# Performance work log

Measured on AMD Instinct MI355X. Metric: run time of the kernel, lower is better.

Reference implementation:

```python
import jax, jax.numpy as jnp
import numpy as np

N, M, D = 50000, 4, 512

def setup_inputs() -> dict:
    key = jax.random.key(0)
    k1, k2, k3, k4 = jax.random.split(key, 4)
    scale = 1.0 / np.sqrt(D)
    return {
        "gnn_output": jax.random.normal(k1, (N, D), dtype=jnp.float32),
        "modality_latents": jax.random.normal(k2, (N, M, D), dtype=jnp.float32),
        "Wq": jax.random.normal(k3, (D, D), dtype=jnp.float32) * scale,
        "bq": jnp.zeros((D,), dtype=jnp.float32),
        "Wk": jax.random.normal(k4, (M, D, D), dtype=jnp.float32) * scale,
        "bk": jnp.zeros((M, D), dtype=jnp.float32),
    }

def reference(gnn_output, modality_latents, Wq, bq, Wk, bk):
    d = modality_latents.shape[-1]
    # query = Linear(gnn_output): torch Linear is x @ W.T + b
    query = gnn_output @ Wq.T + bq                                   # [N, D]
    # all M key projections as one batched GEMM (fused version of the loop)
    keys = jnp.einsum('nmd,med->nme', modality_latents, Wk) + bk     # [N, M, D]
    scores = jnp.einsum('nd,nmd->nm', query, keys) / jnp.sqrt(jnp.float32(d))
    weights = jax.nn.softmax(scores, axis=1)                          # [N, M]
    fused = jnp.einsum('nm,nmd->nd', weights, modality_latents)       # [N, D]
    return (fused, weights)
```

## Files before the change

kernel.cpp:

```cpp
#include <hip/hip_runtime.h>
#include <hip/hip_cooperative_groups.h>

namespace cg = cooperative_groups;


typedef __bf16 bf16x8 __attribute__((ext_vector_type(8)));
typedef __bf16 bf16x4 __attribute__((ext_vector_type(4)));
typedef float  f32x4  __attribute__((ext_vector_type(4)));

#define NTOK 50000
#define DDIM 512
#define NMOD 4
#define BN   32
#define NBLK ((NTOK + BN - 1) / BN)
#define WOFF ((size_t)NTOK * DDIM)
#define GFLOATS 524288
#define TAIL_T 1525
#define SCALE 0.044194173824159216f

#define SWZ(r, b) ((((r) * 1024) + (b)) ^ (((r) & 7) << 4))

__global__ __launch_bounds__(512, 2) void mono_kernel(
    const float* __restrict__ gnn, const float* __restrict__ lat,
    const float* __restrict__ Wq, const float* __restrict__ bq,
    const float* __restrict__ Wk, const float* __restrict__ bk,
    float* __restrict__ out, float* __restrict__ sc, int defer)
{
    __shared__ __align__(16) char smem[35328];
    const int tid = threadIdx.x;
    const int bid = blockIdx.x;
    const int ngrid = gridDim.x;
    cg::grid_group gg = cg::this_grid();

    float* uP = sc + GFLOATS;
    float* vP = uP + 2048;
    float* cP = vP + 2048;
    float* fP = cP + 4;

    {
        float* ldsA = (float*)smem;
        float* ldsB = (float*)(smem + 16384);
        for (int gb = bid; gb < 512; gb += ngrid) {
            const int m = gb >> 7, ib = gb & 127, eblk = ib >> 4, dpb = ib & 15;
            const int el = tid >> 3, c8 = tid & 7;
            f32x4 ac = {0.f, 0.f, 0.f, 0.f};
            for (int r0 = 0; r0 < DDIM; r0 += 64) {
                __syncthreads();
                #pragma unroll
                for (int it = 0; it < 2; ++it) {
                    int idx = it * 512 + tid, r = idx >> 4, c4 = idx & 15;
                    *(f32x4*)&ldsA[r * 64 + c4 * 4] =
                        *(const f32x4*)&Wk[((size_t)m * DDIM + r0 + r) * DDIM + eblk * 64 + c4 * 4];
                }
                {
                    int r = tid >> 3, c4 = tid & 7;
                    *(f32x4*)&ldsB[r * 32 + c4 * 4] =
                        *(const f32x4*)&Wq[(size_t)(r0 + r) * DDIM + dpb * 32 + c4 * 4];
                }
                __syncthreads();
                for (int r = 0; r < 64; ++r) {
                    float wk = ldsA[r * 64 + el];
                    ac += wk * *(const f32x4*)&ldsB[r * 32 + c8 * 4];
                }
            }
            __bf16* Gw = (__bf16*)sc;
            const int eta = eblk * 4 + (el >> 4);
            const int lam = (c8 >> 1) * 16 + (el & 15);
            size_t abf = ((((size_t)m * 16 + dpb) * 32 + eta) * 64 + lam) * 8
                         + (c8 & 1) * 4;
            bf16x4 o;
            o[0] = (__bf16)ac[0]; o[1] = (__bf16)ac[1];
            o[2] = (__bf16)ac[2]; o[3] = (__bf16)ac[3];
            *(bf16x4*)(Gw + abf) = o;
        }

        if (bid < 32) {
            __syncthreads();
            float* up = (float*)smem;
            float* vp = (float*)smem + 256;
            const int m2 = bid >> 3, dc = bid & 7;
            if (tid < 256) {
                const int dl2 = tid & 63, eg = tid >> 6;
                const int d = dc * 64 + dl2;
                float us = 0.f, vs = 0.f;
                #pragma unroll 4
                for (int e = eg * 128; e < eg * 128 + 128; ++e) {
                    us += Wk[((size_t)m2 * DDIM + e) * DDIM + d] * bq[e];
                    vs += Wq[(size_t)e * DDIM + d] * bk[m2 * DDIM + e];
                }
                up[eg * 64 + dl2] = us; vp[eg * 64 + dl2] = vs;
            }
            __syncthreads();
            if (tid < 64) {
                const int d = dc * 64 + tid;
                float uu = up[tid] + up[64+tid] + up[128+tid] + up[192+tid];
                float vv = vp[tid] + vp[64+tid] + vp[128+tid] + vp[192+tid];
                uP[m2 * DDIM + d] = uu;
                vP[m2 * DDIM + d] = vv;
                float cp = 0.f;
                if (dc == 0) {
                    #pragma unroll
                    for (int i = 0; i < 8; ++i)
                        cp += bq[tid * 8 + i] * bk[m2 * DDIM + tid * 8 + i];
                    #pragma unroll
                    for (int msk = 1; msk < 64; msk <<= 1)
                        cp += __shfl_xor(cp, msk, 64);
                    if (tid == 0) cP[m2] = cp;
                }
                unsigned long long anyb =
                    __ballot((uu != 0.f) || (vv != 0.f) || (cp != 0.f));
                if (tid == 0) fP[bid] = anyb ? 1.f : 0.f;
            }
        }
    }
    gg.sync();

    {
        __bf16* tile  = (__bf16*)smem;
        float* s_part = (float*)(smem + 32768);
        f32x4* wlds   = (f32x4*)(smem + 34816);
        const __bf16* Gp = (const __bf16*)sc;
        const int lane = tid & 63, w = tid >> 6;
        const int g = (lane >> 4) & 3, c = lane & 15;

        bool bias = false;
        for (int i2 = 0; i2 < 32; ++i2) bias |= (fP[i2] != 0.f);
        float cm[4];
        #pragma unroll
        for (int m = 0; m < 4; ++m) cm[m] = cP[m];

        for (int t = bid; t < NBLK; t += ngrid) {
            const int row0 = t * BN;
            const int vrows = (NTOK - row0 < BN) ? (NTOK - row0) : BN;

            {
                const float* src = gnn + (size_t)row0 * DDIM;
                #pragma unroll
                for (int i = 0; i < 8; ++i) {
                    int f4 = i * 512 + tid, r = f4 >> 7, c4 = f4 & 127;
                    f32x4 v = (r < vrows)
                        ? __builtin_nontemporal_load(
                              (const f32x4*)(src + (size_t)r * DDIM + c4 * 4))
                        : (f32x4){0.f, 0.f, 0.f, 0.f};
                    bf16x4 o;
                    o[0] = (__bf16)v[0]; o[1] = (__bf16)v[1];
                    o[2] = (__bf16)v[2]; o[3] = (__bf16)v[3];
                    *(bf16x4*)((char*)tile + SWZ(r, c4 * 8)) = o;
                }
            }
            __syncthreads();

            float sm[4];
            for (int m = 0; m < NMOD; ++m) {
                float p[2][4];
                if (bias) {
                    float v4[4];
                    #pragma unroll
                    for (int j = 0; j < 4; ++j)
                        v4[j] = vP[m * DDIM + w * 64 + j * 16 + c];
                    #pragma unroll
                    for (int rt = 0; rt < 2; ++rt)
                        #pragma unroll
                        for (int reg = 0; reg < 4; ++reg) {
                            int r = rt * 16 + g * 4 + reg;
                            float tacc = 0.f;
                            #pragma unroll
                            for (int j = 0; j < 4; ++j) {
                                int col = w * 64 + j * 16 + c;
                                float xv = (float)*(const __bf16*)((const char*)tile +
                                                                   SWZ(r, col * 2));
                                tacc += xv * v4[j];
                            }
                            p[rt][reg] = tacc;
                        }
                } else {
                    #pragma unroll
                    for (int rt = 0; rt < 2; ++rt)
                        #pragma unroll
                        for (int reg = 0; reg < 4; ++reg)
                            p[rt][reg] = 0.f;
                }

                const __bf16* gm = Gp + (size_t)m * 262144;
                #pragma unroll
                for (int jh = 0; jh < 2; ++jh) {
                    float lv[2][2][4];
                    #pragma unroll
                    for (int jj = 0; jj < 2; ++jj) {
                        const int e = w * 64 + (jh * 2 + jj) * 16 + c;
                        #pragma unroll
                        for (int rt = 0; rt < 2; ++rt)
                            #pragma unroll
                            for (int reg = 0; reg < 4; ++reg) {
                                int row = row0 + rt * 16 + g * 4 + reg;
                                lv[jj][rt][reg] = (row < NTOK)
                                    ? lat[((size_t)row * NMOD + m) * DDIM + e]
                                    : 0.f;
                            }
                    }

                    f32x4 kacc[2][2];
                    #pragma unroll
                    for (int rt = 0; rt < 2; ++rt) {
                        kacc[rt][0] = (f32x4){0.f, 0.f, 0.f, 0.f};
                        kacc[rt][1] = (f32x4){0.f, 0.f, 0.f, 0.f};
                    }
                    const __bf16* gpk = gm + (w * 4 + jh * 2) * 512 + lane * 8;
                    #pragma unroll 4
                    for (int kk = 0; kk < 16; ++kk) {
                        bf16x8 b0 = *(const bf16x8*)(gpk + kk * 16384);
                        bf16x8 b1 = *(const bf16x8*)(gpk + kk * 16384 + 512);
                        bf16x8 a[2];
                        const int kb = kk * 64 + g * 16;
                        a[0] = *(const bf16x8*)((const char*)tile + SWZ(c, kb));
                        a[1] = *(const bf16x8*)((const char*)tile + SWZ(16 + c, kb));
                        kacc[0][0] = __builtin_amdgcn_mfma_f32_16x16x32_bf16(
                            a[0], b0, kacc[0][0], 0, 0, 0);
                        kacc[1][0] = __builtin_amdgcn_mfma_f32_16x16x32_bf16(
                            a[1], b0, kacc[1][0], 0, 0, 0);
                        kacc[0][1] = __builtin_amdgcn_mfma_f32_16x16x32_bf16(
                            a[0], b1, kacc[0][1], 0, 0, 0);
                        kacc[1][1] = __builtin_amdgcn_mfma_f32_16x16x32_bf16(
                            a[1], b1, kacc[1][1], 0, 0, 0);
                    }

                    #pragma unroll
                    for (int jj = 0; jj < 2; ++jj) {
                        const int e = w * 64 + (jh * 2 + jj) * 16 + c;
                        float uj = bias ? uP[m * DDIM + e] : 0.f;
                        #pragma unroll
                        for (int rt = 0; rt < 2; ++rt)
                            #pragma unroll
                            for (int reg = 0; reg < 4; ++reg)
                                p[rt][reg] += lv[jj][rt][reg] * (kacc[rt][jj][reg] + uj);
                    }
                    __builtin_amdgcn_sched_barrier(0);
                }

                #pragma unroll
                for (int msk = 1; msk < 16; msk <<= 1)
                    #pragma unroll
                    for (int rt = 0; rt < 2; ++rt)
                        #pragma unroll
                        for (int reg = 0; reg < 4; ++reg)
                            p[rt][reg] += __shfl_xor(p[rt][reg], msk, 64);
                float* sp = s_part + (m & 1) * 256;
                if (c == 0) {
                    #pragma unroll
                    for (int rt = 0; rt < 2; ++rt)
                        #pragma unroll
                        for (int reg = 0; reg < 4; ++reg)
                            sp[w * 32 + rt * 16 + g * 4 + reg] = p[rt][reg];
                }
                __syncthreads();
                if (tid < BN) {
                    float s = 0.f;
                    #pragma unroll
                    for (int ww = 0; ww < 8; ++ww) s += sp[ww * 32 + tid];
                    sm[m] = s + cm[m];
                }
            }

            if (tid < BN) {
                float e0 = __expf(sm[0] * SCALE), e1 = __expf(sm[1] * SCALE),
                      e2 = __expf(sm[2] * SCALE), e3 = __expf(sm[3] * SCALE);
                float iz = 1.f / (e0 + e1 + e2 + e3);
                f32x4 wv = {e0 * iz, e1 * iz, e2 * iz, e3 * iz};
                wlds[tid] = wv;
                if (row0 + tid < NTOK)
                    *(f32x4*)(out + WOFF + (size_t)(row0 + tid) * 4) = wv;
            }
            __syncthreads();

            if (!defer || t < TAIL_T) {
                #pragma unroll 2
                for (int i = 0; i < 8; ++i) {
                    int f4 = i * 512 + tid, r = f4 >> 7, c4 = f4 & 127;
                    if (row0 + r < NTOK) {
                        f32x4 w4 = wlds[r];
                        const float* lp = lat + (size_t)(row0 + r) * NMOD * DDIM + c4 * 4;
                        f32x4 acc = {0.f, 0.f, 0.f, 0.f};
                        #pragma unroll
                        for (int m = 0; m < NMOD; ++m)
                            acc += w4[m] * *(const f32x4*)(lp + m * DDIM);
                        __builtin_nontemporal_store(acc,
                            (f32x4*)(out + (size_t)(row0 + r) * DDIM + c4 * 4));
                    }
                }
            }
        }
    }

    if (defer) {
        gg.sync();
        const long t4 = (long)(NTOK - TAIL_T * BN) * 128;
        for (long idx = (long)bid * 512 + tid; idx < t4;
             idx += (long)ngrid * 512) {
            const int row = TAIL_T * BN + (int)(idx >> 7), c4 = (int)(idx & 127);
            f32x4 w4 = *(const f32x4*)(out + WOFF + (size_t)row * 4);
            f32x4 acc = {0.f, 0.f, 0.f, 0.f};
            #pragma unroll
            for (int m = 0; m < NMOD; ++m) {
                f32x4 v = __builtin_nontemporal_load(
                    (const f32x4*)(lat + ((size_t)row * NMOD + m) * DDIM + c4 * 4));
                acc += w4[m] * v;
            }
            __builtin_nontemporal_store(acc,
                (f32x4*)(out + (size_t)row * DDIM + c4 * 4));
        }
    }
}

extern "C" void kernel_launch(void* const* d_in, const int* in_sizes, int n_in,
                              void* d_out, int out_size, void* d_ws, size_t ws_size,
                              hipStream_t stream)
{
    const float* gnn = (const float*)d_in[0];
    const float* lat = (const float*)d_in[1];
    const float* Wq  = (const float*)d_in[2];
    const float* bq  = (const float*)d_in[3];
    const float* Wk  = (const float*)d_in[4];
    const float* bk  = (const float*)d_in[5];
    float* out = (float*)d_out;

    const size_t need = (size_t)(GFLOATS + 2048 + 2048 + 4 + 32 + 16) * 4;
    float* sc;
    int defer;
    if (ws_size >= need) { sc = (float*)d_ws;      defer = 0; }
    else                 { sc = out + 25000000;    defer = 1; }

    int maxb = 0;
    hipError_t oe = hipOccupancyMaxActiveBlocksPerMultiprocessor(
        &maxb, mono_kernel, 512, 0);
    if (oe != hipSuccess || maxb < 1) maxb = 1;
    if (maxb > 4) maxb = 4;
    const int ngrid = 256 * maxb;

    void* args[] = { (void*)&gnn, (void*)&lat, (void*)&Wq, (void*)&bq,
                     (void*)&Wk, (void*)&bk, (void*)&out, (void*)&sc,
                     (void*)&defer };
    hipLaunchCooperativeKernel((const void*)mono_kernel, dim3(ngrid), dim3(512),
                               args, 0, stream);
}
```

Baseline: 517.2 us.

## Double token tile to 64 rows and use atomic work queue for tiles

Raises the per-block token tile from 32 to 64 rows, so each streamed bf16 weight fragment feeds four MFMA row tiles instead of two, halving global/L2 traffic for the precomputed Wk·Wq matrix per token. Replaces the static strided tile loop with a dynamic atomic counter queue, which balances the load across persistent blocks. In exchange, LDS per block roughly doubles and register pressure grows, which may reduce occupancy under launch_bounds(512,2). The tail-tile count used in defer mode is adjusted to match.

```diff
diff --git a/kernel.cpp b/kernel.cpp
--- a/kernel.cpp
+++ b/kernel.cpp
@@ -11,11 +11,11 @@
 #define NTOK 50000
 #define DDIM 512
 #define NMOD 4
-#define BN   32
+#define BN   64
 #define NBLK ((NTOK + BN - 1) / BN)
 #define WOFF ((size_t)NTOK * DDIM)
 #define GFLOATS 524288
-#define TAIL_T 1525
+#define TAIL_T 762
 #define SCALE 0.044194173824159216f
 
 #define SWZ(r, b) ((((r) * 1024) + (b)) ^ (((r) & 7) << 4))
@@ -26,7 +26,7 @@
     const float* __restrict__ Wk, const float* __restrict__ bk,
     float* __restrict__ out, float* __restrict__ sc, int defer)
 {
-    __shared__ __align__(16) char smem[35328];
+    __shared__ __align__(16) char smem[70720];
     const int tid = threadIdx.x;
     const int bid = blockIdx.x;
     const int ngrid = gridDim.x;
@@ -36,8 +36,10 @@
     float* vP = uP + 2048;
     float* cP = vP + 2048;
     float* fP = cP + 4;
+    int*   qP = (int*)(fP + 32);
 
     {
+        if (bid == 0 && tid == 0) *qP = 0;
         float* ldsA = (float*)smem;
         float* ldsB = (float*)(smem + 16384);
         for (int gb = bid; gb < 512; gb += ngrid) {
@@ -117,8 +119,9 @@
 
     {
         __bf16* tile  = (__bf16*)smem;
-        float* s_part = (float*)(smem + 32768);
-        f32x4* wlds   = (f32x4*)(smem + 34816);
+        float* s_part = (float*)(smem + 65536);
+        f32x4* wlds   = (f32x4*)(smem + 69632);
+        int*   tlds   = (int*)(smem + 70656);
         const __bf16* Gp = (const __bf16*)sc;
         const int lane = tid & 63, w = tid >> 6;
         const int g = (lane >> 4) & 3, c = lane & 15;
@@ -129,14 +132,18 @@
         #pragma unroll
         for (int m = 0; m < 4; ++m) cm[m] = cP[m];
 
-        for (int t = bid; t < NBLK; t += ngrid) {
+        for (;;) {
+            if (tid == 0) *tlds = atomicAdd(qP, 1);
+            __syncthreads();
+            const int t = *tlds;
+            if (t >= NBLK) break;
             const int row0 = t * BN;
             const int vrows = (NTOK - row0 < BN) ? (NTOK - row0) : BN;
 
             {
                 const float* src = gnn + (size_t)row0 * DDIM;
                 #pragma unroll
-                for (int i = 0; i < 8; ++i) {
+                for (int i = 0; i < 16; ++i) {
                     int f4 = i * 512 + tid, r = f4 >> 7, c4 = f4 & 127;
                     f32x4 v = (r < vrows)
                         ? __builtin_nontemporal_load(
@@ -152,14 +159,14 @@
 
             float sm[4];
             for (int m = 0; m < NMOD; ++m) {
-                float p[2][4];
+                float p[4][4];
                 if (bias) {
                     float v4[4];
                     #pragma unroll
                     for (int j = 0; j < 4; ++j)
                         v4[j] = vP[m * DDIM + w * 64 + j * 16 + c];
                     #pragma unroll
-                    for (int rt = 0; rt < 2; ++rt)
+                    for (int rt = 0; rt < 4; ++rt)
                         #pragma unroll
                         for (int reg = 0; reg < 4; ++reg) {
                             int r = rt * 16 + g * 4 + reg;
@@ -175,7 +182,7 @@
                         }
                 } else {
                     #pragma unroll
-                    for (int rt = 0; rt < 2; ++rt)
+                    for (int rt = 0; rt < 4; ++rt)
                         #pragma unroll
                         for (int reg = 0; reg < 4; ++reg)
                             p[rt][reg] = 0.f;
@@ -183,80 +190,68 @@
 
                 const __bf16* gm = Gp + (size_t)m * 262144;
                 #pragma unroll
-                for (int jh = 0; jh < 2; ++jh) {
-                    float lv[2][2][4];
-                    #pragma unroll
-                    for (int jj = 0; jj < 2; ++jj) {
-                        const int e = w * 64 + (jh * 2 + jj) * 16 + c;
-                        #pragma unroll
-                        for (int rt = 0; rt < 2; ++rt)
-                            #pragma unroll
-                            for (int reg = 0; reg < 4; ++reg) {
-                                int row = row0 + rt * 16 + g * 4 + reg;
-                                lv[jj][rt][reg] = (row < NTOK)
-                                    ? lat[((size_t)row * NMOD + m) * DDIM + e]
-                                    : 0.f;
-                            }
+                for (int jp = 0; jp < 4; ++jp) {
+                    const int e = w * 64 + jp * 16 + c;
+                    float lv[4][4];
+                    #pragma unroll
+                    for (int rt = 0; rt < 4; ++rt)
+                        #pragma unroll
+                        for (int reg = 0; reg < 4; ++reg) {
+                            int row = row0 + rt * 16 + g * 4 + reg;
+                            lv[rt][reg] = (row < NTOK)
+                                ? lat[((size_t)row * NMOD + m) * DDIM + e]
+                                : 0.f;
+                        }
+
+                    f32x4 kacc[4];
+                    #pragma unroll
+                    for (int rt = 0; rt < 4; ++rt)
+                        kacc[rt] = (f32x4){0.f, 0.f, 0.f, 0.f};
+                    const __bf16* gpk = gm + (w * 4 + jp) * 512 + lane * 8;
+                    #pragma unroll 2
+                    for (int kk = 0; kk < 16; ++kk) {
+                        bf16x8 b = *(const bf16x8*)(gpk + (size_t)kk * 16384);
+                        bf16x8 a[4];
+                        const int kb = kk * 64 + g * 16;
+                        #pragma unroll
+                        for (int rt = 0; rt < 4; ++rt)
+                            a[rt] = *(const bf16x8*)((const char*)tile +
+                                                     SWZ(rt * 16 + c, kb));
+                        #pragma unroll
+                        for (int rt = 0; rt < 4; ++rt)
+                            kacc[rt] = __builtin_amdgcn_mfma_f32_16x16x32_bf16(
+                                a[rt], b, kacc[rt], 0, 0, 0);
                     }
 
-                    f32x4 kacc[2][2];
-                    #pragma unroll
-                    for (int rt = 0; rt < 2; ++rt) {
-                        kacc[rt][0] = (f32x4){0.f, 0.f, 0.f, 0.f};
-                        kacc[rt][1] = (f32x4){0.f, 0.f, 0.f, 0.f};
-                    }
-                    const __bf16* gpk = gm + (w * 4 + jh * 2) * 512 + lane * 8;
-                    #pragma unroll 4
-                    for (int kk = 0; kk < 16; ++kk) {
-                        bf16x8 b0 = *(const bf16x8*)(gpk + kk * 16384);
-                        bf16x8 b1 = *(const bf16x8*)(gpk + kk * 16384 + 512);
-                        bf16x8 a[2];
-                        const int kb = kk * 64 + g * 16;
-                        a[0] = *(const bf16x8*)((const char*)tile + SWZ(c, kb));
-                        a[1] = *(const bf16x8*)((const char*)tile + SWZ(16 + c, kb));
-                        kacc[0][0] = __builtin_amdgcn_mfma_f32_16x16x32_bf16(
-                            a[0], b0, kacc[0][0], 0, 0, 0);
-                        kacc[1][0] = __builtin_amdgcn_mfma_f32_16x16x32_bf16(
-                            a[1], b0, kacc[1][0], 0, 0, 0);
-                        kacc[0][1] = __builtin_amdgcn_mfma_f32_16x16x32_bf16(
-                            a[0], b1, kacc[0][1], 0, 0, 0);
-                        kacc[1][1] = __builtin_amdgcn_mfma_f32_16x16x32_bf16(
-                            a[1], b1, kacc[1][1], 0, 0, 0);
-                    }
-
-                    #pragma unroll
-                    for (int jj = 0; jj < 2; ++jj) {
-                        const int e = w * 64 + (jh * 2 + jj) * 16 + c;
-                        float uj = bias ? uP[m * DDIM + e] : 0.f;
-                        #pragma unroll
-                        for (int rt = 0; rt < 2; ++rt)
-                            #pragma unroll
-                            for (int reg = 0; reg < 4; ++reg)
-                                p[rt][reg] += lv[jj][rt][reg] * (kacc[rt][jj][reg] + uj);
-                    }
+                    float uj = bias ? uP[m * DDIM + e] : 0.f;
+                    #pragma unroll
+                    for (int rt = 0; rt < 4; ++rt)
+                        #pragma unroll
+                        for (int reg = 0; reg < 4; ++reg)
+                            p[rt][reg] += lv[rt][reg] * (kacc[rt][reg] + uj);
                     __builtin_amdgcn_sched_barrier(0);
                 }
 
                 #pragma unroll
                 for (int msk = 1; msk < 16; msk <<= 1)
                     #pragma unroll
-                    for (int rt = 0; rt < 2; ++rt)
+                    for (int rt = 0; rt < 4; ++rt)
                         #pragma unroll
                         for (int reg = 0; reg < 4; ++reg)
                             p[rt][reg] += __shfl_xor(p[rt][reg], msk, 64);
-                float* sp = s_part + (m & 1) * 256;
+                float* sp = s_part + (m & 1) * 512;
                 if (c == 0) {
                     #pragma unroll
-                    for (int rt = 0; rt < 2; ++rt)
+                    for (int rt = 0; rt < 4; ++rt)
                         #pragma unroll
                         for (int reg = 0; reg < 4; ++reg)
-                            sp[w * 32 + rt * 16 + g * 4 + reg] = p[rt][reg];
+                            sp[w * 64 + rt * 16 + g * 4 + reg] = p[rt][reg];
                 }
                 __syncthreads();
                 if (tid < BN) {
                     float s = 0.f;
                     #pragma unroll
-                    for (int ww = 0; ww < 8; ++ww) s += sp[ww * 32 + tid];
+                    for (int ww = 0; ww < 8; ++ww) s += sp[ww * 64 + tid];
                     sm[m] = s + cm[m];
                 }
             }
@@ -274,7 +269,7 @@
 
             if (!defer || t < TAIL_T) {
                 #pragma unroll 2
-                for (int i = 0; i < 8; ++i) {
+                for (int i = 0; i < 16; ++i) {
                     int f4 = i * 512 + tid, r = f4 >> 7, c4 = f4 & 127;
                     if (row0 + r < NTOK) {
                         f32x4 w4 = wlds[r];
@@ -323,7 +318,7 @@
     const float* bk  = (const float*)d_in[5];
     float* out = (float*)d_out;
 
-    const size_t need = (size_t)(GFLOATS + 2048 + 2048 + 4 + 32 + 16) * 4;
+    const size_t need = (size_t)(GFLOATS + 2048 + 2048 + 4 + 32 + 64) * 4;
     float* sc;
     int defer;
     if (ws_size >= need) { sc = (float*)d_ws;      defer = 0; }
```

Measured after the change: 602.9 us. +16.6%, slower.
